# Kernel tuning notes

Measured on AMD Instinct MI355X. Metric: run time of the kernel, lower is better.

Reference implementation:

```python
import jax, jax.numpy as jnp
import numpy as np

HIDDEN = 256
HEADS = 4
N_CHECKINS = 500000
N_POIS = 50000


def setup_inputs() -> dict:
    key = jax.random.key(0)
    ks = jax.random.split(key, 12)
    lim = 1.0 / np.sqrt(HIDDEN)
    def lin(k):
        kw, kb = jax.random.split(k)
        W = jax.random.uniform(kw, (HIDDEN, HIDDEN), jnp.float32, -lim, lim)
        b = jax.random.uniform(kb, (HIDDEN,), jnp.float32, -lim, lim)
        return W, b
    Wq, bq = lin(ks[0]); Wk, bk = lin(ks[1]); Wv, bv = lin(ks[2]); Wo, bo = lin(ks[3])
    # xavier_uniform for S [1, hidden]: gain=1, fan_in=hidden, fan_out=1
    a = np.sqrt(6.0 / (HIDDEN + 1))
    S = jax.random.uniform(ks[4], (1, HIDDEN), jnp.float32, -a, a)
    prelu_a = jnp.float32(0.25)  # PReLU default init
    x = jax.random.normal(ks[5], (N_CHECKINS, HIDDEN), jnp.float32)
    checkin_to_poi = jax.random.randint(ks[6], (N_CHECKINS,), 0, N_POIS, jnp.int64 if jax.config.jax_enable_x64 else jnp.int32)
    return {"x": x, "checkin_to_poi": checkin_to_poi, "num_pois": N_POIS,
            "Wq": Wq, "bq": bq, "Wk": Wk, "bk": bk, "Wv": Wv, "bv": bv,
            "Wo": Wo, "bo": bo, "S": S, "prelu_a": prelu_a}


def reference(x, checkin_to_poi, num_pois, Wq, bq, Wk, bk, Wv, bv, Wo, bo, S, prelu_a):
    C = x.shape[1]
    H = HEADS
    d = C // H
    idx = checkin_to_poi
    K = x @ Wk.T + bk                      # [N, C]
    V = x @ Wv.T + bv                      # [N, C]
    Q = S @ Wq.T + bq                      # [1, C]
    Ks = K.reshape(-1, H, d)
    Vs = V.reshape(-1, H, d)
    Qs = Q.reshape(1, H, d)
    scale = jnp.sqrt(jnp.float32(C))
    scores = (Ks * Qs).sum(-1) / scale     # [N, H]
    # segment softmax over POI groups (pyg_softmax)
    smax = jax.ops.segment_max(scores, idx, num_segments=num_pois)  # [P, H]
    smax = jnp.where(jnp.isfinite(smax), smax, 0.0)  # empty segments -> -inf -> 0
    e = jnp.exp(scores - smax[idx])
    denom = jax.ops.segment_sum(e, idx, num_segments=num_pois)      # [P, H]
    alpha = e / (denom[idx] + 1e-16)       # [N, H]
    weighted_V = Vs * alpha[..., None]     # [N, H, d]
    poi_agg = jax.ops.segment_sum(weighted_V.reshape(-1, C), idx, num_segments=num_pois)  # [P, C]
    O = Q + poi_agg                        # broadcast Q over POIs
    O = O + jax.nn.relu(O @ Wo.T + bo)
    O = jnp.where(O >= 0, O, prelu_a * O)  # PReLU (single shared parameter)
    return jnp.nan_to_num(O, nan=0.0)
```

## Files before the change

### kernel.cpp

```cpp
#include <hip/hip_runtime.h>
#include <stdint.h>

typedef __bf16 bf16x8 __attribute__((ext_vector_type(8)));
typedef float f32x4 __attribute__((ext_vector_type(4)));

#define MFMA16(A, B, C) __builtin_amdgcn_mfma_f32_16x16x32_bf16((A), (B), (C), 0, 0, 0)

__device__ __forceinline__ float b2f(unsigned short u) {
    union { unsigned int i; float f; } v; v.i = ((unsigned int)u) << 16; return v.f;
}
__device__ __forceinline__ unsigned short f2b(float f) {
    union { float f; unsigned int i; } v; v.f = f;
    unsigned int x = v.i;
    return (unsigned short)((x + 0x7FFFu + ((x >> 16) & 1u)) >> 16);
}
__device__ __forceinline__ float ldf(const void* p, long i, int isbf) {
    return isbf ? b2f(((const unsigned short*)p)[i]) : ((const float*)p)[i];
}

__global__ void k_probe(const unsigned int* __restrict__ wq,
                        const unsigned int* __restrict__ idxw, int* __restrict__ flags) {
    if (threadIdx.x == 0) {
        int ok = 0;
        for (int i = 0; i < 8; i++) {
            unsigned int e = (wq[i] >> 7) & 0xFFu;
            if (e >= 0x60u && e <= 0x7Cu) ok++;
        }
        flags[0] = (ok == 8) ? 1 : 0;
        int z = 0, lr = 0;
        for (int i = 0; i < 4; i++) {
            if (idxw[2 * i + 1] == 0u) z++;
            if (idxw[2 * i] < 0x4000000u) lr++;
        }
        flags[1] = (z == 4 && lr == 4) ? 1 : 0;
    }
}

__global__ void k_q(const void* __restrict__ S, const void* __restrict__ Wq,
                    const void* __restrict__ bq, const void* __restrict__ prelu,
                    const int* __restrict__ flags, float* __restrict__ Q,
                    float* __restrict__ pf) {
    int isbf = flags[0];
    int c = threadIdx.x;
    float acc = 0.f;
    for (int j = 0; j < 256; j++) acc += ldf(S, j, isbf) * ldf(Wq, (long)c * 256 + j, isbf);
    Q[c] = acc + ldf(bq, c, isbf);
    if (c == 0)
        pf[0] = isbf ? b2f(((const unsigned short*)prelu)[0]) : ((const float*)prelu)[0];
}

__global__ void k_qk(const void* __restrict__ Wk, const void* __restrict__ bk,
                     const float* __restrict__ Q, const int* __restrict__ flags,
                     unsigned short* __restrict__ qkb, float* __restrict__ qb) {
    int isbf = flags[0];
    int h = blockIdx.x, j = threadIdx.x;
    float acc = 0.f;
    if (h < 4) {
        for (int d = 0; d < 64; d++) acc += ldf(Wk, (long)(h * 64 + d) * 256 + j, isbf) * Q[h * 64 + d];
        acc *= 0.0625f;
    }
    qkb[h * 256 + j] = f2b(acc);
    if (j == 0) {
        float s = 0.f;
        if (h < 4) {
            for (int d = 0; d < 64; d++) s += ldf(bk, h * 64 + d, isbf) * Q[h * 64 + d];
            s *= 0.0625f;
        }
        qb[h] = s;
    }
}

__global__ void k_cvt(const void* __restrict__ Wv, const void* __restrict__ Wo,
                      const int* __restrict__ flags, unsigned short* __restrict__ Wvb,
                      unsigned short* __restrict__ Wob) {
    int isbf = flags[0];
    long i = (long)blockIdx.x * 256 + threadIdx.x;
    const void* src = (i < 65536) ? Wv : Wo;
    unsigned short* dst = (i < 65536) ? Wvb : Wob;
    long k = (i < 65536) ? i : i - 65536;
    dst[k] = isbf ? ((const unsigned short*)src)[k] : f2b(((const float*)src)[k]);
}


__global__ void k_hist(const int* __restrict__ idxp, const int* __restrict__ flags,
                       int* __restrict__ counts, int N) {
    int is64 = flags[1];
    int i = blockIdx.x * 256 + threadIdx.x;
    if (i < N) {
        int p = is64 ? idxp[(long)i << 1] : idxp[i];
        atomicAdd(&counts[p], 1);
    }
}

__global__ __launch_bounds__(256) void k_scan1(const int* __restrict__ counts,
                                               int* __restrict__ offs,
                                               int* __restrict__ bsum, int P) {
    __shared__ int sh[256];
    int t = threadIdx.x;
    int i = blockIdx.x * 256 + t;
    int v = (i < P) ? counts[i] : 0;
    int s = v;
    sh[t] = s;
    __syncthreads();
    for (int d = 1; d < 256; d <<= 1) {
        int add = (t >= d) ? sh[t - d] : 0;
        __syncthreads();
        s += add;
        sh[t] = s;
        __syncthreads();
    }
    if (i < P) offs[i] = s - v;
    if (t == 255) bsum[blockIdx.x] = s;
}

__global__ __launch_bounds__(256) void k_scan2(int* __restrict__ bsum, int nb) {
    __shared__ int sh[256];
    int t = threadIdx.x;
    int K = (nb + 255) / 256;
    int j0 = t * K;
    int local = 0;
    for (int k = 0; k < K; k++) {
        int j = j0 + k;
        if (j < nb) local += bsum[j];
    }
    int s = local;
    sh[t] = s;
    __syncthreads();
    for (int d = 1; d < 256; d <<= 1) {
        int add = (t >= d) ? sh[t - d] : 0;
        __syncthreads();
        s += add;
        sh[t] = s;
        __syncthreads();
    }
    int run = s - local;
    for (int k = 0; k < K; k++) {
        int j = j0 + k;
        if (j < nb) { int tmp = bsum[j]; bsum[j] = run; run += tmp; }
    }
}

__global__ void k_scan3(int* __restrict__ offs, const int* __restrict__ bsum, int P) {
    int i = blockIdx.x * 256 + threadIdx.x;
    if (i < P) offs[i] += bsum[blockIdx.x];
}

__global__ void k_scatter(const int* __restrict__ idxp, const int* __restrict__ flags,
                          const int* __restrict__ offs, int* __restrict__ cursor,
                          int* __restrict__ order, int* __restrict__ pois, int N) {
    int is64 = flags[1];
    int i = blockIdx.x * 256 + threadIdx.x;
    if (i < N) {
        int p = is64 ? idxp[(long)i << 1] : idxp[i];
        int pos = atomicAdd(&cursor[p], 1);
        int j = offs[p] + pos;
        order[j] = i;
        pois[j] = p;
    }
}

__global__ __launch_bounds__(256) void k_v(
    const void* __restrict__ x, const int* __restrict__ order,
    const int* __restrict__ pois,
    const unsigned short* __restrict__ Wvb, const unsigned short* __restrict__ qkb,
    const float* __restrict__ qb, const int* __restrict__ flags,
    float* __restrict__ denom, float* __restrict__ vagg, int N) {
    __shared__ unsigned short xs[128 * 264];
    __shared__ float es[128][4];
    int isbf = flags[0];
    int tid = threadIdx.x;
    long base = (long)blockIdx.x * 128;

#pragma unroll
    for (int ch = 0; ch < 16; ch++) {
        int i16 = tid + ch * 256;
        int row = i16 >> 5;
        int col = (i16 & 31) * 8;
        long grow = base + row;
        uint4 t;
        if (grow < N) {
            long n = (long)order[grow];
            if (isbf) {
                t = *(const uint4*)((const unsigned short*)x + n * 256 + col);
            } else {
                const float* xp = (const float*)x + n * 256 + col;
                float4 a = *(const float4*)xp;
                float4 b = *(const float4*)(xp + 4);
                t.x = (unsigned int)f2b(a.x) | ((unsigned int)f2b(a.y) << 16);
                t.y = (unsigned int)f2b(a.z) | ((unsigned int)f2b(a.w) << 16);
                t.z = (unsigned int)f2b(b.x) | ((unsigned int)f2b(b.y) << 16);
                t.w = (unsigned int)f2b(b.z) | ((unsigned int)f2b(b.w) << 16);
            }
        } else {
            t.x = t.y = t.z = t.w = 0u;
        }
        *(uint4*)&xs[row * 264 + col] = t;
    }
    __syncthreads();

    int w = tid >> 6, l = tid & 63;
    int m = l & 15, q = l >> 4;

    int ids[2][4];
#pragma unroll
    for (int g2 = 0; g2 < 2; g2++)
#pragma unroll
        for (int r = 0; r < 4; r++) {
            long gr = base + w * 32 + g2 * 16 + q * 4 + r;
            ids[g2][r] = (gr < N) ? pois[gr] : -1;
        }

    bf16x8 a[2][8];
#pragma unroll
    for (int g2 = 0; g2 < 2; g2++)
#pragma unroll
        for (int s = 0; s < 8; s++)
            a[g2][s] = *(const bf16x8*)&xs[(w * 32 + g2 * 16 + m) * 264 + q * 8 + s * 32];

    {
        const bf16x8* qkp = (const bf16x8*)(qkb + (size_t)m * 256);
        bf16x8 qf[8];
#pragma unroll
        for (int s = 0; s < 8; s++) qf[s] = qkp[q + s * 4];
        float qbm = qb[m & 3];
#pragma unroll
        for (int g2 = 0; g2 < 2; g2++) {
            f32x4 sacc = {0.f, 0.f, 0.f, 0.f};
#pragma unroll
            for (int s = 0; s < 8; s++) sacc = MFMA16(a[g2][s], qf[s], sacc);
            if (m < 4) {
                int rid = -1;
                float run = 0.f;
#pragma unroll
                for (int r = 0; r < 4; r++) {
                    int row = w * 32 + g2 * 16 + q * 4 + r;
                    long gr = base + row;
                    float e = 0.f;
                    if (gr < N) e = __expf(sacc[r] + qbm);
                    es[row][m] = e;
                    int id = ids[g2][r];
                    if (id == rid) {
                        run += e;
                    } else {
                        if (rid >= 0) unsafeAtomicAdd(&denom[(long)rid * 4 + m], run);
                        rid = id;
                        run = e;
                    }
                }
                if (rid >= 0) unsafeAtomicAdd(&denom[(long)rid * 4 + m], run);
            }
        }
    }

#pragma unroll 1
    for (int t = 0; t < 16; t++) {
        int h_t = t >> 2;
        const bf16x8* wvp = (const bf16x8*)(Wvb + (size_t)(t * 16 + m) * 256);
        bf16x8 b[8];
#pragma unroll
        for (int s = 0; s < 8; s++) b[s] = wvp[q + s * 4];
#pragma unroll
        for (int g2 = 0; g2 < 2; g2++) {
            f32x4 acc = {0.f, 0.f, 0.f, 0.f};
#pragma unroll
            for (int s = 0; s < 8; s++) acc = MFMA16(a[g2][s], b[s], acc);
            int rid = -1;
            float run = 0.f;
#pragma unroll
            for (int r = 0; r < 4; r++) {
                int row = w * 32 + g2 * 16 + q * 4 + r;
                float val = acc[r] * es[row][h_t];
                int id = ids[g2][r];
                if (id == rid) {
                    run += val;
                } else {
                    if (rid >= 0) unsafeAtomicAdd(&vagg[(long)rid * 256 + t * 16 + m], run);
                    rid = id;
                    run = val;
                }
            }
            if (rid >= 0) unsafeAtomicAdd(&vagg[(long)rid * 256 + t * 16 + m], run);
        }
    }
}

__global__ __launch_bounds__(256) void k_out(
    const float* __restrict__ Q, const float* __restrict__ denom,
    const float* __restrict__ vagg, const void* __restrict__ bv,
    const unsigned short* __restrict__ Wob, const void* __restrict__ bo,
    const float* __restrict__ pf, const int* __restrict__ flags,
    void* __restrict__ out, int P) {
    __shared__ float Os[4][16 * 264];
    int isbf = flags[0];
    int tid = threadIdx.x;
    int w = tid >> 6, l = tid & 63;
    int m = l & 15, q = l >> 4;
    long pbase = (long)blockIdx.x * 64 + w * 16;
    float aP = pf[0];
    long pm = pbase + m;
    bool vm = pm < P;

    float den4[4], rd4[4];
#pragma unroll
    for (int h = 0; h < 4; h++) {
        float d = vm ? denom[pm * 4 + h] : 0.f;
        den4[h] = d;
        rd4[h] = 1.0f / (d + 1e-16f);
    }

    bf16x8 of[8];
#pragma unroll
    for (int s = 0; s < 8; s++) {
        int c0 = q * 8 + s * 32;
        int h = s >> 1;
        bf16x8 ov;
        if (vm) {
            const float* ag = vagg + pm * 256 + c0;
#pragma unroll
            for (int j = 0; j < 8; j++) {
                float o = Q[c0 + j] + (ag[j] + ldf(bv, c0 + j, isbf) * den4[h]) * rd4[h];
                Os[w][m * 264 + c0 + j] = o;
                ov[j] = (__bf16)o;
            }
        } else {
#pragma unroll
            for (int j = 0; j < 8; j++) { Os[w][m * 264 + c0 + j] = 0.f; ov[j] = (__bf16)0.0f; }
        }
        of[s] = ov;
    }

#pragma unroll 1
    for (int t = 0; t < 16; t++) {
        const bf16x8* wop = (const bf16x8*)(Wob + (size_t)(t * 16 + m) * 256);
        f32x4 acc = {0.f, 0.f, 0.f, 0.f};
#pragma unroll
        for (int s = 0; s < 8; s++) acc = MFMA16(of[s], wop[q + s * 4], acc);
        int c = t * 16 + m;
        float boc = ldf(bo, c, isbf);
#pragma unroll
        for (int r = 0; r < 4; r++) {
            int row = q * 4 + r;
            long p = pbase + row;
            if (p < P) {
                float Ov = Os[w][row * 264 + c];
                float lin = fmaxf(acc[r] + boc, 0.f);
                float res = Ov + lin;
                res = (res >= 0.f) ? res : aP * res;
                if (res != res) res = 0.f;
                if (isbf) ((unsigned short*)out)[p * 256 + c] = f2b(res);
                else      ((float*)out)[p * 256 + c] = res;
            }
        }
    }
}

extern "C" void kernel_launch(void* const* d_in, const int* in_sizes, int n_in,
                              void* d_out, int out_size, void* d_ws, size_t ws_size,
                              hipStream_t stream) {
    const void* x  = d_in[0];
    const int* idx = (const int*)d_in[1];
    const void* Wq = d_in[3];
    const void* bq = d_in[4];
    const void* Wk = d_in[5];
    const void* bk = d_in[6];
    const void* Wv = d_in[7];
    const void* bv = d_in[8];
    const void* Wo = d_in[9];
    const void* bo = d_in[10];
    const void* S  = d_in[11];
    const void* pr = d_in[12];

    int N = in_sizes[0] / 256;
    int P = out_size / 256;
    int nb1 = (P + 255) / 256;
    int nbN = (N + 255) / 256;

    float* ws = (float*)d_ws;
    int* flags          = (int*)ws;
    float* pf           = ws + 2;
    float* Q            = ws + 16;
    float* qb           = ws + 272;
    unsigned short* qkb = (unsigned short*)(ws + 288);
    unsigned short* Wvb = (unsigned short*)(ws + 2336);
    unsigned short* Wob = (unsigned short*)(ws + 35104);
    float* denom        = ws + 67872;
    float* vagg         = denom + (size_t)P * 4;

    int* counts = (int*)vagg;
    int* cursor = counts + P;
    int* offs   = cursor + P;
    int* bsum   = offs + P;

    int* order  = (int*)(vagg + (size_t)P * 256);
    int* pois   = order + N;

    size_t need = (67872 + (size_t)P * 260) * sizeof(float) + (size_t)2 * N * sizeof(int);
    if (ws_size < need) return;

    hipMemsetAsync(counts, 0, (size_t)2 * P * sizeof(int), stream);

    k_probe<<<1, 64, 0, stream>>>((const unsigned int*)Wq, (const unsigned int*)idx, flags);
    k_q<<<1, 256, 0, stream>>>(S, Wq, bq, pr, flags, Q, pf);
    k_qk<<<16, 256, 0, stream>>>(Wk, bk, Q, flags, qkb, qb);
    k_cvt<<<512, 256, 0, stream>>>(Wv, Wo, flags, Wvb, Wob);

    k_hist<<<nbN, 256, 0, stream>>>(idx, flags, counts, N);
    k_scan1<<<nb1, 256, 0, stream>>>(counts, offs, bsum, P);
    k_scan2<<<1, 256, 0, stream>>>(bsum, nb1);
    k_scan3<<<nb1, 256, 0, stream>>>(offs, bsum, P);
    k_scatter<<<nbN, 256, 0, stream>>>(idx, flags, offs, cursor, order, pois, N);

    hipMemsetAsync(denom, 0, (size_t)P * 260 * sizeof(float), stream);

    k_v<<<(N + 127) / 128, 256, 0, stream>>>(x, order, pois, Wvb, qkb, qb, flags, denom, vagg, N);
    k_out<<<(P + 63) / 64, 256, 0, stream>>>(Q, denom, vagg, bv, Wob, bo, pf, flags, d_out, P);
}
```

Measured before the change: 1.260 ms.

## Reduce POI segments in LDS and store interior segments without atomics

Result: faster. 1.133 ms (-10.1%).

```diff
diff --git a/kernel.cpp b/kernel.cpp
--- a/kernel.cpp
+++ b/kernel.cpp
@@ -36,38 +36,48 @@
     }
 }
 
-__global__ void k_q(const void* __restrict__ S, const void* __restrict__ Wq,
-                    const void* __restrict__ bq, const void* __restrict__ prelu,
-                    const int* __restrict__ flags, float* __restrict__ Q,
-                    float* __restrict__ pf) {
+__global__ __launch_bounds__(256) void k_qk(
+    const void* __restrict__ S, const void* __restrict__ Wq, const void* __restrict__ bq,
+    const void* __restrict__ Wk, const void* __restrict__ bk, const void* __restrict__ prelu,
+    const int* __restrict__ flags, float* __restrict__ Q,
+    unsigned short* __restrict__ qkb, float* __restrict__ qb, float* __restrict__ pf) {
+    __shared__ float Qh[64];
+    __shared__ float part[256];
     int isbf = flags[0];
-    int c = threadIdx.x;
-    float acc = 0.f;
-    for (int j = 0; j < 256; j++) acc += ldf(S, j, isbf) * ldf(Wq, (long)c * 256 + j, isbf);
-    Q[c] = acc + ldf(bq, c, isbf);
-    if (c == 0)
-        pf[0] = isbf ? b2f(((const unsigned short*)prelu)[0]) : ((const float*)prelu)[0];
-}
-
-__global__ void k_qk(const void* __restrict__ Wk, const void* __restrict__ bk,
-                     const float* __restrict__ Q, const int* __restrict__ flags,
-                     unsigned short* __restrict__ qkb, float* __restrict__ qb) {
-    int isbf = flags[0];
-    int h = blockIdx.x, j = threadIdx.x;
+    int h = blockIdx.x, tid = threadIdx.x;
+    if (h < 4) {
+        int d = tid >> 2, quad = tid & 3;
+        float ps = 0.f;
+        for (int j = 0; j < 64; j++)
+            ps += ldf(S, quad * 64 + j, isbf) *
+                  ldf(Wq, (long)(h * 64 + d) * 256 + quad * 64 + j, isbf);
+        part[tid] = ps;
+        __syncthreads();
+        if (quad == 0) {
+            float qv = part[tid] + part[tid + 1] + part[tid + 2] + part[tid + 3] +
+                       ldf(bq, h * 64 + d, isbf);
+            Qh[d] = qv;
+            Q[h * 64 + d] = qv;
+        }
+        __syncthreads();
+    }
+    int j = tid;
     float acc = 0.f;
     if (h < 4) {
-        for (int d = 0; d < 64; d++) acc += ldf(Wk, (long)(h * 64 + d) * 256 + j, isbf) * Q[h * 64 + d];
+        for (int d = 0; d < 64; d++) acc += ldf(Wk, (long)(h * 64 + d) * 256 + j, isbf) * Qh[d];
         acc *= 0.0625f;
     }
     qkb[h * 256 + j] = f2b(acc);
     if (j == 0) {
         float s = 0.f;
         if (h < 4) {
-            for (int d = 0; d < 64; d++) s += ldf(bk, h * 64 + d, isbf) * Q[h * 64 + d];
+            for (int d = 0; d < 64; d++) s += ldf(bk, h * 64 + d, isbf) * Qh[d];
             s *= 0.0625f;
         }
         qb[h] = s;
     }
+    if (h == 0 && j == 0)
+        pf[0] = isbf ? b2f(((const unsigned short*)prelu)[0]) : ((const float*)prelu)[0];
 }
 
 __global__ void k_cvt(const void* __restrict__ Wv, const void* __restrict__ Wo,
@@ -147,75 +157,80 @@
 
 __global__ void k_scatter(const int* __restrict__ idxp, const int* __restrict__ flags,
                           const int* __restrict__ offs, int* __restrict__ cursor,
-                          int* __restrict__ order, int* __restrict__ pois, int N) {
+                          int2* __restrict__ op, int N) {
     int is64 = flags[1];
     int i = blockIdx.x * 256 + threadIdx.x;
     if (i < N) {
         int p = is64 ? idxp[(long)i << 1] : idxp[i];
         int pos = atomicAdd(&cursor[p], 1);
-        int j = offs[p] + pos;
-        order[j] = i;
-        pois[j] = p;
+        op[offs[p] + pos] = make_int2(i, p);
     }
 }
 
 __global__ __launch_bounds__(256) void k_v(
-    const void* __restrict__ x, const int* __restrict__ order,
-    const int* __restrict__ pois,
+    const void* __restrict__ x, const int2* __restrict__ op,
     const unsigned short* __restrict__ Wvb, const unsigned short* __restrict__ qkb,
     const float* __restrict__ qb, const int* __restrict__ flags,
     float* __restrict__ denom, float* __restrict__ vagg, int N) {
-    __shared__ unsigned short xs[128 * 264];
+    __shared__ float vt[2][128][17];
     __shared__ float es[128][4];
+    __shared__ int prow[128];
+    __shared__ int segstart[129];
+    __shared__ int segpoi[128];
+    __shared__ int wtot[4];
+    __shared__ int sm[4];
     int isbf = flags[0];
     int tid = threadIdx.x;
     long base = (long)blockIdx.x * 128;
-
-#pragma unroll
-    for (int ch = 0; ch < 16; ch++) {
-        int i16 = tid + ch * 256;
-        int row = i16 >> 5;
-        int col = (i16 & 31) * 8;
-        long grow = base + row;
-        uint4 t;
-        if (grow < N) {
-            long n = (long)order[grow];
-            if (isbf) {
-                t = *(const uint4*)((const unsigned short*)x + n * 256 + col);
-            } else {
-                const float* xp = (const float*)x + n * 256 + col;
-                float4 a = *(const float4*)xp;
-                float4 b = *(const float4*)(xp + 4);
-                t.x = (unsigned int)f2b(a.x) | ((unsigned int)f2b(a.y) << 16);
-                t.y = (unsigned int)f2b(a.z) | ((unsigned int)f2b(a.w) << 16);
-                t.z = (unsigned int)f2b(b.x) | ((unsigned int)f2b(b.y) << 16);
-                t.w = (unsigned int)f2b(b.z) | ((unsigned int)f2b(b.w) << 16);
-            }
-        } else {
-            t.x = t.y = t.z = t.w = 0u;
-        }
-        *(uint4*)&xs[row * 264 + col] = t;
-    }
+    long rem = (long)N - base;
+    int nv = (rem < 128) ? (int)rem : 128;
+
+    if (tid < 128) prow[tid] = (tid < nv) ? op[base + tid].y : -1;
     __syncthreads();
+    bool bnd = (tid < 128) && (tid < nv) && (tid == 0 || prow[tid] != prow[tid - 1]);
+    unsigned long long mask = __ballot(bnd);
+    if ((tid & 63) == 0) wtot[tid >> 6] = __popcll(mask);
+    __syncthreads();
+    int ns = wtot[0] + wtot[1];
+    if (bnd) {
+        int s = __popcll(mask & ((1ull << (tid & 63)) - 1)) + ((tid >= 64) ? wtot[0] : 0);
+        segstart[s] = tid;
+        segpoi[s] = prow[tid];
+    }
+    if (tid == 0) {
+        segstart[ns] = nv;
+        int pv = 0, nx = 0;
+        if (base > 0 && op[base - 1].y == prow[0]) pv = 1;
+        if (base + nv < (long)N && op[base + nv].y == prow[nv - 1]) nx = 1;
+        sm[1] = pv;
+        sm[2] = nx;
+    }
 
     int w = tid >> 6, l = tid & 63;
     int m = l & 15, q = l >> 4;
 
-    int ids[2][4];
-#pragma unroll
-    for (int g2 = 0; g2 < 2; g2++)
-#pragma unroll
-        for (int r = 0; r < 4; r++) {
-            long gr = base + w * 32 + g2 * 16 + q * 4 + r;
-            ids[g2][r] = (gr < N) ? pois[gr] : -1;
-        }
-
     bf16x8 a[2][8];
 #pragma unroll
-    for (int g2 = 0; g2 < 2; g2++)
-#pragma unroll
-        for (int s = 0; s < 8; s++)
-            a[g2][s] = *(const bf16x8*)&xs[(w * 32 + g2 * 16 + m) * 264 + q * 8 + s * 32];
+    for (int g2 = 0; g2 < 2; g2++) {
+        long gr = base + w * 32 + g2 * 16 + m;
+        long n = (gr < N) ? (long)op[gr].x : 0;
+        if (isbf) {
+            const unsigned short* xb = (const unsigned short*)x + n * 256 + q * 8;
+#pragma unroll
+            for (int s = 0; s < 8; s++) a[g2][s] = *(const bf16x8*)(xb + s * 32);
+        } else {
+            const float* xf = (const float*)x + n * 256 + q * 8;
+#pragma unroll
+            for (int s = 0; s < 8; s++) {
+                float4 lo = *(const float4*)(xf + s * 32);
+                float4 hi = *(const float4*)(xf + s * 32 + 4);
+                bf16x8 t;
+                t[0] = (__bf16)lo.x; t[1] = (__bf16)lo.y; t[2] = (__bf16)lo.z; t[3] = (__bf16)lo.w;
+                t[4] = (__bf16)hi.x; t[5] = (__bf16)hi.y; t[6] = (__bf16)hi.z; t[7] = (__bf16)hi.w;
+                a[g2][s] = t;
+            }
+        }
+    }
 
     {
         const bf16x8* qkp = (const bf16x8*)(qkb + (size_t)m * 256);
@@ -229,8 +244,6 @@
 #pragma unroll
             for (int s = 0; s < 8; s++) sacc = MFMA16(a[g2][s], qf[s], sacc);
             if (m < 4) {
-                int rid = -1;
-                float run = 0.f;
 #pragma unroll
                 for (int r = 0; r < 4; r++) {
                     int row = w * 32 + g2 * 16 + q * 4 + r;
@@ -238,23 +251,30 @@
                     float e = 0.f;
                     if (gr < N) e = __expf(sacc[r] + qbm);
                     es[row][m] = e;
-                    int id = ids[g2][r];
-                    if (id == rid) {
-                        run += e;
-                    } else {
-                        if (rid >= 0) unsafeAtomicAdd(&denom[(long)rid * 4 + m], run);
-                        rid = id;
-                        run = e;
-                    }
                 }
-                if (rid >= 0) unsafeAtomicAdd(&denom[(long)rid * 4 + m], run);
-            }
+            }
+        }
+    }
+    __syncthreads();
+
+    int pv = sm[1], nx = sm[2];
+
+    {
+        int c = tid & 3, s0 = tid >> 2;
+        for (int s = s0; s < ns; s += 64) {
+            int r0 = segstart[s], r1 = segstart[s + 1];
+            float sum = 0.f;
+            for (int r = r0; r < r1; r++) sum += es[r][c];
+            float* dst = &denom[(long)segpoi[s] * 4 + c];
+            if ((s == 0 && pv) || (s == ns - 1 && nx)) unsafeAtomicAdd(dst, sum);
+            else *dst = sum;
         }
     }
 
 #pragma unroll 1
     for (int t = 0; t < 16; t++) {
         int h_t = t >> 2;
+        int buf = t & 1;
         const bf16x8* wvp = (const bf16x8*)(Wvb + (size_t)(t * 16 + m) * 256);
         bf16x8 b[8];
 #pragma unroll
@@ -264,22 +284,23 @@
             f32x4 acc = {0.f, 0.f, 0.f, 0.f};
 #pragma unroll
             for (int s = 0; s < 8; s++) acc = MFMA16(a[g2][s], b[s], acc);
-            int rid = -1;
-            float run = 0.f;
 #pragma unroll
             for (int r = 0; r < 4; r++) {
                 int row = w * 32 + g2 * 16 + q * 4 + r;
-                float val = acc[r] * es[row][h_t];
-                int id = ids[g2][r];
-                if (id == rid) {
-                    run += val;
-                } else {
-                    if (rid >= 0) unsafeAtomicAdd(&vagg[(long)rid * 256 + t * 16 + m], run);
-                    rid = id;
-                    run = val;
-                }
-            }
-            if (rid >= 0) unsafeAtomicAdd(&vagg[(long)rid * 256 + t * 16 + m], run);
+                vt[buf][row][m] = acc[r] * es[row][h_t];
+            }
+        }
+        __syncthreads();
+        {
+            int c = tid & 15, s0 = tid >> 4;
+            for (int s = s0; s < ns; s += 16) {
+                int r0 = segstart[s], r1 = segstart[s + 1];
+                float sum = 0.f;
+                for (int r = r0; r < r1; r++) sum += vt[buf][r][c];
+                float* dst = &vagg[(long)segpoi[s] * 256 + t * 16 + c];
+                if ((s == 0 && pv) || (s == ns - 1 && nx)) unsafeAtomicAdd(dst, sum);
+                else *dst = sum;
+            }
         }
     }
 }
@@ -391,8 +412,7 @@
     int* offs   = cursor + P;
     int* bsum   = offs + P;
 
-    int* order  = (int*)(vagg + (size_t)P * 256);
-    int* pois   = order + N;
+    int2* op = (int2*)(vagg + (size_t)P * 256);
 
     size_t need = (67872 + (size_t)P * 260) * sizeof(float) + (size_t)2 * N * sizeof(int);
     if (ws_size < need) return;
@@ -400,18 +420,17 @@
     hipMemsetAsync(counts, 0, (size_t)2 * P * sizeof(int), stream);
 
     k_probe<<<1, 64, 0, stream>>>((const unsigned int*)Wq, (const unsigned int*)idx, flags);
-    k_q<<<1, 256, 0, stream>>>(S, Wq, bq, pr, flags, Q, pf);
-    k_qk<<<16, 256, 0, stream>>>(Wk, bk, Q, flags, qkb, qb);
+    k_qk<<<16, 256, 0, stream>>>(S, Wq, bq, Wk, bk, pr, flags, Q, qkb, qb, pf);
     k_cvt<<<512, 256, 0, stream>>>(Wv, Wo, flags, Wvb, Wob);
 
     k_hist<<<nbN, 256, 0, stream>>>(idx, flags, counts, N);
     k_scan1<<<nb1, 256, 0, stream>>>(counts, offs, bsum, P);
     k_scan2<<<1, 256, 0, stream>>>(bsum, nb1);
     k_scan3<<<nb1, 256, 0, stream>>>(offs, bsum, P);
-    k_scatter<<<nbN, 256, 0, stream>>>(idx, flags, offs, cursor, order, pois, N);
+    k_scatter<<<nbN, 256, 0, stream>>>(idx, flags, offs, cursor, op, N);
 
     hipMemsetAsync(denom, 0, (size_t)P * 260 * sizeof(float), stream);
 
-    k_v<<<(N + 127) / 128, 256, 0, stream>>>(x, order, pois, Wvb, qkb, qb, flags, denom, vagg, N);
+    k_v<<<(N + 127) / 128, 256, 0, stream>>>(x, op, Wvb, qkb, qb, flags, denom, vagg, N);
     k_out<<<(P + 63) / 64, 256, 0, stream>>>(Q, denom, vagg, bv, Wob, bo, pf, flags, d_out, P);
 }
```
